# Optimization experiments

Hardware: AMD Instinct MI355X
Metric: run time of the kernel (lower is better)

Reference implementation:

```python
import jax, jax.numpy as jnp
import numpy as np

N = 100000      # nodes
E = 1600000     # edges (before self-loops)
IN = 128        # in_channels
H = 4           # heads
C = 32          # hidden_channels (per head)
HC = H * C      # 128, LayerNorm dim
NEG_SLOPE = 0.2
LN_EPS = 1e-5


def setup_inputs() -> dict:
    key = jax.random.key(0)
    ks = jax.random.split(key, 8)
    x = jax.random.normal(ks[0], (N, IN), dtype=jnp.float32)
    edge_index = jax.random.randint(ks[1], (2, E), 0, N, dtype=jnp.int64)
    edge_weight = jax.random.uniform(ks[2], (E,), dtype=jnp.float32)
    # GATConv parameters
    W = jax.random.normal(ks[3], (IN, HC), dtype=jnp.float32) * (1.0 / np.sqrt(IN))
    att_src = jax.random.normal(ks[4], (H, C), dtype=jnp.float32) * (1.0 / np.sqrt(C))
    att_dst = jax.random.normal(ks[5], (H, C), dtype=jnp.float32) * (1.0 / np.sqrt(C))
    bias = jnp.zeros((HC,), dtype=jnp.float32)
    # LayerNorm parameters
    gamma = jnp.ones((HC,), dtype=jnp.float32)
    beta = jnp.zeros((HC,), dtype=jnp.float32)
    return {"x": x, "edge_index": edge_index, "edge_weight": edge_weight,
            "W": W, "att_src": att_src, "att_dst": att_dst, "bias": bias,
            "gamma": gamma, "beta": beta}


def reference(x, edge_index, edge_weight, W, att_src, att_dst, bias, gamma, beta):
    # --- GATConv (heads=4, concat, add_self_loops=True) ---
    loops = jnp.arange(N, dtype=edge_index.dtype)
    ei = jnp.concatenate([edge_index, jnp.stack([loops, loops])], axis=1)  # [2, E+N]
    src, dst = ei[0], ei[1]

    xw = (x @ W).reshape(N, H, C)                       # [N, H, C]
    a_src = jnp.sum(xw * att_src, axis=-1)              # [N, H]
    a_dst = jnp.sum(xw * att_dst, axis=-1)              # [N, H]

    # per-edge attention logits, softmax grouped by destination node
    e = jax.nn.leaky_relu(a_src[src] + a_dst[dst], NEG_SLOPE)   # [E+N, H]
    m = jax.ops.segment_max(e, dst, num_segments=N)             # [N, H]
    ex = jnp.exp(e - m[dst])
    denom = jax.ops.segment_sum(ex, dst, num_segments=N)        # [N, H]
    alpha = ex / (denom[dst] + 1e-16)                           # [E+N, H]

    # weighted scatter-add of source features to destinations
    msg = alpha[:, :, None] * xw[src]                           # [E+N, H, C]
    out = jax.ops.segment_sum(msg, dst, num_segments=N)         # [N, H, C]
    out = out.reshape(N, HC) + bias                             # concat heads + bias

    # --- LayerNorm ---
    mu = jnp.mean(out, axis=-1, keepdims=True)
    var = jnp.var(out, axis=-1, keepdims=True)
    return gamma * (out - mu) / jnp.sqrt(var + LN_EPS) + beta
```

## Files before the change

### kernel.cpp

```cpp
#include <hip/hip_runtime.h>
#include <math.h>

#define NN 100000
#define EE 1600000
#define ETOT (EE + NN)
#define NBUK 512
#define NPB 196
#define CHUNK 3125
#define CAP 6144
#define GB 1563

typedef __attribute__((ext_vector_type(8))) short bf16x8;
typedef __attribute__((ext_vector_type(4))) float f32x4;

__device__ __forceinline__ unsigned short f2bf(float f) {
  unsigned int u = __float_as_uint(f);
  u = u + 0x7fffu + ((u >> 16) & 1u);
  return (unsigned short)(u >> 16);
}

__device__ __forceinline__ float lrelu_exp(float e) {
  e = (e > 0.f) ? e : 0.2f * e;
  return __expf(e);
}

__global__ __launch_bounds__(256) void k_gemm(const float* __restrict__ x,
                                              const float* __restrict__ W,
                                              const float* __restrict__ att_src,
                                              const float* __restrict__ att_dst,
                                              const int* __restrict__ ei,
                                              unsigned short* __restrict__ xwb,
                                              float* __restrict__ asrc,
                                              float* __restrict__ adst,
                                              int* __restrict__ H) {
  __shared__ __align__(16) unsigned short lds[17408];
  __shared__ float satt[256];
  __shared__ int hh[NBUK];
  int tid = threadIdx.x;

  if (blockIdx.x >= GB) {
    int j = blockIdx.x - GB;
    for (int i = tid; i < NBUK; i += 256) hh[i] = 0;
    __syncthreads();
    int e0 = j * CHUNK;
    for (int e = e0 + tid; e < e0 + CHUNK; e += 256) {
      int d = ei[(size_t)EE + e];
      atomicAdd(&hh[d / NPB], 1);
    }
    __syncthreads();
    for (int i = tid; i < NBUK; i += 256) H[j * NBUK + i] = hh[i];
    return;
  }

  for (int i = tid; i < 16384; i += 256) {
    int k = i >> 7, n = i & 127;
    lds[n * 136 + k] = f2bf(W[i]);
  }
  if (tid < 128) satt[tid] = att_src[tid];
  else satt[tid] = att_dst[tid - 128];
  __syncthreads();

  int wv = tid >> 6, lane = tid & 63;
  int m = lane & 15, q = lane >> 4;
  int r = blockIdx.x * 64 + wv * 16 + m;
  bool rok = (r < NN);

  bf16x8 af[4];
#pragma unroll
  for (int kt = 0; kt < 4; kt++) {
    float4 v0 = make_float4(0.f, 0.f, 0.f, 0.f), v1 = v0;
    if (rok) {
      v0 = ((const float4*)x)[(size_t)r * 32 + kt * 8 + q * 2];
      v1 = ((const float4*)x)[(size_t)r * 32 + kt * 8 + q * 2 + 1];
    }
    af[kt][0] = (short)f2bf(v0.x); af[kt][1] = (short)f2bf(v0.y);
    af[kt][2] = (short)f2bf(v0.z); af[kt][3] = (short)f2bf(v0.w);
    af[kt][4] = (short)f2bf(v1.x); af[kt][5] = (short)f2bf(v1.y);
    af[kt][6] = (short)f2bf(v1.z); af[kt][7] = (short)f2bf(v1.w);
  }

  f32x4 acc[8];
#pragma unroll
  for (int nt = 0; nt < 8; nt++) acc[nt] = (f32x4){0.f, 0.f, 0.f, 0.f};

#pragma unroll
  for (int nt = 0; nt < 8; nt++) {
#pragma unroll
    for (int kt = 0; kt < 4; kt++) {
      bf16x8 bf = *((const bf16x8*)&lds[(nt * 16 + m) * 136 + kt * 32 + q * 8]);
      acc[nt] = __builtin_amdgcn_mfma_f32_16x16x32_bf16(af[kt], bf, acc[nt], 0, 0, 0);
    }
  }

  __syncthreads();
#pragma unroll
  for (int nt = 0; nt < 8; nt++)
#pragma unroll
    for (int rg = 0; rg < 4; rg++)
      lds[(wv * 16 + q * 4 + rg) * 128 + nt * 16 + m] = f2bf(acc[nt][rg]);
  __syncthreads();

  size_t base = (size_t)blockIdx.x * 16384;
  const size_t lim = (size_t)NN * 256;
  for (int i = tid; i < 1024; i += 256) {
    size_t off = base + (size_t)i * 16;
    if (off < lim) *((uint4*)((char*)xwb + off)) = ((const uint4*)lds)[i];
  }

  int row = tid >> 2, h = tid & 3;
  int node = blockIdx.x * 64 + row;
  if (node < NN) {
    float ss = 0.f, sd = 0.f;
#pragma unroll
    for (int cq = 0; cq < 4; cq++) {
      uint4 u = *((const uint4*)&lds[row * 128 + h * 32 + cq * 8]);
      int cb = h * 32 + cq * 8;
      float f0 = __uint_as_float(u.x << 16), f1 = __uint_as_float(u.x & 0xffff0000u);
      float f2 = __uint_as_float(u.y << 16), f3 = __uint_as_float(u.y & 0xffff0000u);
      float f4 = __uint_as_float(u.z << 16), f5 = __uint_as_float(u.z & 0xffff0000u);
      float f6 = __uint_as_float(u.w << 16), f7 = __uint_as_float(u.w & 0xffff0000u);
      ss += f0 * satt[cb] + f1 * satt[cb + 1] + f2 * satt[cb + 2] + f3 * satt[cb + 3] +
            f4 * satt[cb + 4] + f5 * satt[cb + 5] + f6 * satt[cb + 6] + f7 * satt[cb + 7];
      sd += f0 * satt[128 + cb] + f1 * satt[128 + cb + 1] + f2 * satt[128 + cb + 2] +
            f3 * satt[128 + cb + 3] + f4 * satt[128 + cb + 4] + f5 * satt[128 + cb + 5] +
            f6 * satt[128 + cb + 6] + f7 * satt[128 + cb + 7];
    }
    asrc[(size_t)node * 4 + h] = ss;
    adst[(size_t)node * 4 + h] = sd;
  }
}

__global__ __launch_bounds__(512) void k_s1(const int* __restrict__ H,
                                            int* __restrict__ R, int* __restrict__ T) {
  __shared__ int s[512];
  int b = blockIdx.x, t = threadIdx.x;
  int v = H[t * NBUK + b];
  s[t] = v;
  __syncthreads();
  for (int off = 1; off < 512; off <<= 1) {
    int tmp = (t >= off) ? s[t - off] : 0;
    __syncthreads();
    s[t] += tmp;
    __syncthreads();
  }
  R[b * 512 + t] = s[t] - v;
  if (t == 511) T[b] = s[511];
}

__global__ __launch_bounds__(512) void k_s2(const int* __restrict__ T,
                                            int* __restrict__ BaseTmp,
                                            int* __restrict__ Base) {
  __shared__ int s[512];
  __shared__ int s2[512];
  int t = threadIdx.x;
  int v = T[t];
  int ncnt = NN - t * NPB;
  ncnt = (ncnt < 0) ? 0 : ((ncnt > NPB) ? NPB : ncnt);
  int w = v + ncnt;
  s[t] = v; s2[t] = w;
  __syncthreads();
  for (int off = 1; off < 512; off <<= 1) {
    int ta = (t >= off) ? s[t - off] : 0;
    int tb = (t >= off) ? s2[t - off] : 0;
    __syncthreads();
    s[t] += ta; s2[t] += tb;
    __syncthreads();
  }
  BaseTmp[t] = s[t] - v;
  Base[t] = s2[t] - w;
}

__global__ __launch_bounds__(256) void k_p3(const int* __restrict__ ei,
                                            const int* __restrict__ R,
                                            const int* __restrict__ BaseTmp,
                                            int* __restrict__ tmpb) {
  __shared__ int cur[NBUK];
  int j = blockIdx.x, t = threadIdx.x;
  for (int b = t; b < NBUK; b += 256) cur[b] = BaseTmp[b] + R[b * 512 + j];
  __syncthreads();
  int e0 = j * CHUNK;
  for (int e = e0 + t; e < e0 + CHUNK; e += 256) {
    int s = ei[e];
    int d = ei[(size_t)EE + e];
    int b = d / NPB;
    int li = d - b * NPB;
    int pos = atomicAdd(&cur[b], 1);
    tmpb[pos] = (li << 17) | s;
  }
}

__global__ __launch_bounds__(256) void k_p4(const int* __restrict__ tmpb,
                                            const int* __restrict__ T,
                                            const int* __restrict__ BaseTmp,
                                            const int* __restrict__ Base,
                                            int* __restrict__ es, int* __restrict__ offs) {
  __shared__ int cnt[256];
  __shared__ int cur[NPB];
  __shared__ int stage[CAP];
  int b = blockIdx.x, t = threadIdx.x;
  if (b == 0 && t == 0) offs[NN] = ETOT;
  int n0 = b * NPB;
  int nloc = NN - n0;
  if (nloc <= 0) return;
  if (nloc > NPB) nloc = NPB;
  int total = T[b];
  int bt = BaseTmp[b], bs = Base[b];
  cnt[t] = (t < nloc) ? 1 : 0;
  __syncthreads();
  for (int e = t; e < total; e += 256) {
    int u = tmpb[bt + e];
    atomicAdd(&cnt[u >> 17], 1);
  }
  __syncthreads();
  int v = cnt[t];
  __syncthreads();
  for (int off = 1; off < 256; off <<= 1) {
    int tmp = (t >= off) ? cnt[t - off] : 0;
    __syncthreads();
    cnt[t] += tmp;
    __syncthreads();
  }
  int excl = cnt[t] - v;
  if (t < nloc) {
    offs[n0 + t] = bs + excl;
    cur[t] = excl + 1;
    if (excl < CAP) stage[excl] = n0 + t;
  }
  __syncthreads();
  for (int e = t; e < total; e += 256) {
    int u = tmpb[bt + e];
    int pos = atomicAdd(&cur[u >> 17], 1);
    if (pos < CAP) stage[pos] = u & 0x1FFFF;
  }
  __syncthreads();
  int btot = total + nloc;
  if (btot > CAP) btot = CAP;
  for (int i = t; i < btot; i += 256) es[bs + i] = stage[i];
}

__global__ __launch_bounds__(256) void k_agg(const unsigned short* __restrict__ xwb,
                                             const float* __restrict__ asrc,
                                             const float* __restrict__ adst,
                                             const int* __restrict__ offs,
                                             const int* __restrict__ es,
                                             const float* __restrict__ bias,
                                             const float* __restrict__ gamma,
                                             const float* __restrict__ beta,
                                             float* __restrict__ out) {
  int lane = threadIdx.x & 63;
  int node = blockIdx.x * 4 + (threadIdx.x >> 6);
  int off0 = offs[node];
  int d = offs[node + 1] - off0;
  int h = lane >> 4;
  int he = lane & 3;
  int sel = lane >> 3;
  int c = lane * 2;

  float4 ad4 = *((const float4*)(adst + (size_t)node * 4));
  float ade = (he & 2) ? ((he & 1) ? ad4.w : ad4.z) : ((he & 1) ? ad4.y : ad4.x);

  const unsigned* xp = (const unsigned*)xwb + lane;
  const int* ep = es + off0;
  float ax0 = 0.f, ay0 = 0.f, ax1 = 0.f, ay1 = 0.f;
  float wsum = 0.f;

  int nb = (d + 7) >> 3;
  int4 sa = *((const int4*)(ep));
  int4 sb = *((const int4*)(ep + 4));

  for (int b = 0; b < nb; ++b) {
    int4 na = *((const int4*)(ep + (b + 1) * 8));
    int4 nbv = *((const int4*)(ep + (b + 1) * 8 + 4));

    int base = b * 8;
    int s0 = sa.x, s1 = sa.y, s2 = sa.z, s3 = sa.w;
    int s4 = sb.x, s5 = sb.y, s6 = sb.z, s7 = sb.w;
    bool full = (base + 8 <= d);
    if (!full) {
      s0 = (base + 0 < d) ? s0 : 0; s1 = (base + 1 < d) ? s1 : 0;
      s2 = (base + 2 < d) ? s2 : 0; s3 = (base + 3 < d) ? s3 : 0;
      s4 = (base + 4 < d) ? s4 : 0; s5 = (base + 5 < d) ? s5 : 0;
      s6 = (base + 6 < d) ? s6 : 0; s7 = (base + 7 < d) ? s7 : 0;
    }
    int t0 = (sel & 1) ? s1 : s0;
    int t1 = (sel & 1) ? s3 : s2;
    int t2 = (sel & 1) ? s5 : s4;
    int t3 = (sel & 1) ? s7 : s6;
    int p0 = (sel & 2) ? t1 : t0;
    int p1 = (sel & 2) ? t3 : t2;
    int se = (sel & 4) ? p1 : p0;
    float av = asrc[(size_t)(unsigned)se * 4u + (unsigned)he];

    unsigned u0 = xp[(unsigned)s0 * 64u];
    unsigned u1 = xp[(unsigned)s1 * 64u];
    unsigned u2 = xp[(unsigned)s2 * 64u];
    unsigned u3 = xp[(unsigned)s3 * 64u];
    unsigned u4 = xp[(unsigned)s4 * 64u];
    unsigned u5 = xp[(unsigned)s5 * 64u];
    unsigned u6 = xp[(unsigned)s6 * 64u];
    unsigned u7 = xp[(unsigned)s7 * 64u];

    float wl = lrelu_exp(av + ade);
    float w0 = __shfl(wl, 0 * 8 + h);
    float w1 = __shfl(wl, 1 * 8 + h);
    float w2 = __shfl(wl, 2 * 8 + h);
    float w3 = __shfl(wl, 3 * 8 + h);
    float w4 = __shfl(wl, 4 * 8 + h);
    float w5 = __shfl(wl, 5 * 8 + h);
    float w6 = __shfl(wl, 6 * 8 + h);
    float w7 = __shfl(wl, 7 * 8 + h);
    if (!full) {
      w0 = (base + 0 < d) ? w0 : 0.f; w1 = (base + 1 < d) ? w1 : 0.f;
      w2 = (base + 2 < d) ? w2 : 0.f; w3 = (base + 3 < d) ? w3 : 0.f;
      w4 = (base + 4 < d) ? w4 : 0.f; w5 = (base + 5 < d) ? w5 : 0.f;
      w6 = (base + 6 < d) ? w6 : 0.f; w7 = (base + 7 < d) ? w7 : 0.f;
    }
    wsum += ((w0 + w1) + (w2 + w3)) + ((w4 + w5) + (w6 + w7));
    ax0 = fmaf(w0, __uint_as_float(u0 << 16), ax0);
    ay0 = fmaf(w0, __uint_as_float(u0 & 0xffff0000u), ay0);
    ax1 = fmaf(w1, __uint_as_float(u1 << 16), ax1);
    ay1 = fmaf(w1, __uint_as_float(u1 & 0xffff0000u), ay1);
    ax0 = fmaf(w2, __uint_as_float(u2 << 16), ax0);
    ay0 = fmaf(w2, __uint_as_float(u2 & 0xffff0000u), ay0);
    ax1 = fmaf(w3, __uint_as_float(u3 << 16), ax1);
    ay1 = fmaf(w3, __uint_as_float(u3 & 0xffff0000u), ay1);
    ax0 = fmaf(w4, __uint_as_float(u4 << 16), ax0);
    ay0 = fmaf(w4, __uint_as_float(u4 & 0xffff0000u), ay0);
    ax1 = fmaf(w5, __uint_as_float(u5 << 16), ax1);
    ay1 = fmaf(w5, __uint_as_float(u5 & 0xffff0000u), ay1);
    ax0 = fmaf(w6, __uint_as_float(u6 << 16), ax0);
    ay0 = fmaf(w6, __uint_as_float(u6 & 0xffff0000u), ay0);
    ax1 = fmaf(w7, __uint_as_float(u7 << 16), ax1);
    ay1 = fmaf(w7, __uint_as_float(u7 & 0xffff0000u), ay1);

    sa = na; sb = nbv;
  }

  float accx = ax0 + ax1, accy = ay0 + ay1;
  float rn = 1.f / (wsum + 1e-16f);

  float vx = accx * rn + bias[c];
  float vy = accy * rn + bias[c + 1];
  float sum = vx + vy, sq = vx * vx + vy * vy;
#pragma unroll
  for (int o = 32; o; o >>= 1) {
    sum += __shfl_xor(sum, o);
    sq += __shfl_xor(sq, o);
  }
  float mean = sum * (1.f / 128.f);
  float var = sq * (1.f / 128.f) - mean * mean;
  float rs = rsqrtf(var + 1e-5f);
  float o0 = gamma[c] * (vx - mean) * rs + beta[c];
  float o1 = gamma[c + 1] * (vy - mean) * rs + beta[c + 1];
  float2 ov; ov.x = o0; ov.y = o1;
  *((float2*)(out + (size_t)node * 128 + c)) = ov;
}

extern "C" void kernel_launch(void* const* d_in, const int* in_sizes, int n_in,
                              void* d_out, int out_size, void* d_ws, size_t ws_size,
                              hipStream_t stream) {
  const float* x = (const float*)d_in[0];
  const int* ei = (const int*)d_in[1];
  const float* W = (const float*)d_in[3];
  const float* att_src = (const float*)d_in[4];
  const float* att_dst = (const float*)d_in[5];
  const float* bias = (const float*)d_in[6];
  const float* gamma = (const float*)d_in[7];
  const float* beta = (const float*)d_in[8];
  float* out = (float*)d_out;

  char* p = (char*)d_ws;
  auto alloc = [&](size_t bytes) -> char* {
    char* r = p;
    p += (bytes + 255) & ~(size_t)255;
    return r;
  };
  unsigned short* xwb = (unsigned short*)alloc((size_t)NN * 128 * 2);
  float* asrc = (float*)alloc((size_t)NN * 4 * 4);
  float* adst = (float*)alloc((size_t)NN * 4 * 4);
  int* es = (int*)alloc((size_t)ETOT * 4 + 128);
  int* offs = (int*)alloc((size_t)(NN + 1) * 4);
  int* tmpb = (int*)alloc((size_t)EE * 4);
  int* H = (int*)alloc((size_t)512 * NBUK * 4);
  int* R = (int*)alloc((size_t)NBUK * 512 * 4);
  int* T = (int*)alloc((size_t)NBUK * 4);
  int* BaseTmp = (int*)alloc((size_t)(NBUK + 1) * 4);
  int* Base = (int*)alloc((size_t)(NBUK + 1) * 4);

  k_gemm<<<GB + NBUK, 256, 0, stream>>>(x, W, att_src, att_dst, ei, xwb, asrc, adst, H);
  k_s1<<<NBUK, 512, 0, stream>>>(H, R, T);
  k_s2<<<1, 512, 0, stream>>>(T, BaseTmp, Base);
  k_p3<<<512, 256, 0, stream>>>(ei, R, BaseTmp, tmpb);
  k_p4<<<NBUK, 256, 0, stream>>>(tmpb, T, BaseTmp, Base, es, offs);
  k_agg<<<NN / 4, 256, 0, stream>>>(xwb, asrc, adst, offs, es, bias, gamma, beta, out);
}
```

Baseline: 255.2 us.

## Fuse CSR build stages into GEMM kernel with grid-wide atomic barriers

Merges the histogram, two scan kernels, bucket scatter and per-bucket sort into the GEMM launch. The first 512 blocks act as persistent workers that synchronise through global atomic counters, while the remaining blocks run the GEMM concurrently. This removes four kernel launches and lets the CSR construction overlap the matmul. It risks deadlock if the 512 worker blocks are not all co-resident, and adds spin-wait overhead plus a memset.

Result: slower. 633.7 us (+148.3%).

```diff
diff --git a/kernel.cpp b/kernel.cpp
--- a/kernel.cpp
+++ b/kernel.cpp
@@ -8,6 +8,7 @@
 #define NPB 196
 #define CHUNK 3125
 #define CAP 6144
+#define CB 512
 #define GB 1563
 
 typedef __attribute__((ext_vector_type(8))) short bf16x8;
@@ -24,7 +25,22 @@
   return __expf(e);
 }
 
-__global__ __launch_bounds__(256) void k_gemm(const float* __restrict__ x,
+__device__ __forceinline__ void arrive_cnt(int* c) {
+  __threadfence();
+  __syncthreads();
+  if (threadIdx.x == 0)
+    __hip_atomic_fetch_add(c, 1, __ATOMIC_RELAXED, __HIP_MEMORY_SCOPE_AGENT);
+}
+__device__ __forceinline__ void wait_cnt(int* c, int target) {
+  if (threadIdx.x == 0) {
+    while (__hip_atomic_load(c, __ATOMIC_RELAXED, __HIP_MEMORY_SCOPE_AGENT) < target)
+      __builtin_amdgcn_s_sleep(2);
+  }
+  __syncthreads();
+  __threadfence();
+}
+
+__global__ __launch_bounds__(256) void k_mega(const float* __restrict__ x,
                                               const float* __restrict__ W,
                                               const float* __restrict__ att_src,
                                               const float* __restrict__ att_dst,
@@ -32,26 +48,178 @@
                                               unsigned short* __restrict__ xwb,
                                               float* __restrict__ asrc,
                                               float* __restrict__ adst,
-                                              int* __restrict__ H) {
+                                              int* __restrict__ H, int* __restrict__ R,
+                                              int* __restrict__ T,
+                                              int* __restrict__ BaseTmp,
+                                              int* __restrict__ Base,
+                                              int* __restrict__ tmpb,
+                                              int* __restrict__ es, int* __restrict__ offs,
+                                              int* __restrict__ sync) {
   __shared__ __align__(16) unsigned short lds[17408];
   __shared__ float satt[256];
-  __shared__ int hh[NBUK];
   int tid = threadIdx.x;
-
-  if (blockIdx.x >= GB) {
-    int j = blockIdx.x - GB;
-    for (int i = tid; i < NBUK; i += 256) hh[i] = 0;
+  int* ish = (int*)lds;
+
+  if (blockIdx.x < CB) {
+    int j = blockIdx.x;
+    for (int i = tid; i < NBUK; i += 256) ish[i] = 0;
     __syncthreads();
     int e0 = j * CHUNK;
     for (int e = e0 + tid; e < e0 + CHUNK; e += 256) {
       int d = ei[(size_t)EE + e];
-      atomicAdd(&hh[d / NPB], 1);
+      atomicAdd(&ish[d / NPB], 1);
     }
     __syncthreads();
-    for (int i = tid; i < NBUK; i += 256) H[j * NBUK + i] = hh[i];
+    for (int i = tid; i < NBUK; i += 256) H[j * NBUK + i] = ish[i];
+    arrive_cnt(&sync[0]);
+    wait_cnt(&sync[0], CB);
+
+    {
+      int* s = ish;
+      int va = H[tid * NBUK + j];
+      int vb = H[(tid + 256) * NBUK + j];
+      s[tid] = va;
+      __syncthreads();
+      for (int off = 1; off < 256; off <<= 1) {
+        int tmp = (tid >= off) ? s[tid - off] : 0;
+        __syncthreads();
+        s[tid] += tmp;
+        __syncthreads();
+      }
+      int Sa = s[tid], SaT = s[255];
+      __syncthreads();
+      s[tid] = vb;
+      __syncthreads();
+      for (int off = 1; off < 256; off <<= 1) {
+        int tmp = (tid >= off) ? s[tid - off] : 0;
+        __syncthreads();
+        s[tid] += tmp;
+        __syncthreads();
+      }
+      int Sb = s[tid];
+      R[j * 512 + tid] = Sa - va;
+      R[j * 512 + 256 + tid] = SaT + Sb - vb;
+      if (tid == 255) T[j] = SaT + Sb;
+    }
+    arrive_cnt(&sync[1]);
+
+    if (j == 0) {
+      wait_cnt(&sync[1], CB);
+      int* s = ish;
+      int e2 = tid + 256;
+      int v1 = T[tid], v2 = T[e2];
+      int nc1 = NN - tid * NPB; nc1 = nc1 < 0 ? 0 : (nc1 > NPB ? NPB : nc1);
+      int nc2 = NN - e2 * NPB;  nc2 = nc2 < 0 ? 0 : (nc2 > NPB ? NPB : nc2);
+      int w1 = v1 + nc1, w2 = v2 + nc2;
+      s[tid] = v1;
+      __syncthreads();
+      for (int off = 1; off < 256; off <<= 1) {
+        int tmp = (tid >= off) ? s[tid - off] : 0;
+        __syncthreads();
+        s[tid] += tmp;
+        __syncthreads();
+      }
+      int Sa = s[tid], SaT = s[255];
+      __syncthreads();
+      s[tid] = v2;
+      __syncthreads();
+      for (int off = 1; off < 256; off <<= 1) {
+        int tmp = (tid >= off) ? s[tid - off] : 0;
+        __syncthreads();
+        s[tid] += tmp;
+        __syncthreads();
+      }
+      BaseTmp[tid] = Sa - v1;
+      BaseTmp[e2] = SaT + s[tid] - v2;
+      __syncthreads();
+      s[tid] = w1;
+      __syncthreads();
+      for (int off = 1; off < 256; off <<= 1) {
+        int tmp = (tid >= off) ? s[tid - off] : 0;
+        __syncthreads();
+        s[tid] += tmp;
+        __syncthreads();
+      }
+      int Sc = s[tid], ScT = s[255];
+      __syncthreads();
+      s[tid] = w2;
+      __syncthreads();
+      for (int off = 1; off < 256; off <<= 1) {
+        int tmp = (tid >= off) ? s[tid - off] : 0;
+        __syncthreads();
+        s[tid] += tmp;
+        __syncthreads();
+      }
+      Base[tid] = Sc - w1;
+      Base[e2] = ScT + s[tid] - w2;
+      arrive_cnt(&sync[2]);
+    }
+    wait_cnt(&sync[2], 1);
+
+    {
+      int* cur = ish;
+      for (int b2 = tid; b2 < NBUK; b2 += 256) cur[b2] = BaseTmp[b2] + R[b2 * 512 + j];
+      __syncthreads();
+      for (int e = e0 + tid; e < e0 + CHUNK; e += 256) {
+        int sv = ei[e];
+        int dv = ei[(size_t)EE + e];
+        int b2 = dv / NPB;
+        int li = dv - b2 * NPB;
+        int pos = atomicAdd(&cur[b2], 1);
+        tmpb[pos] = (li << 17) | sv;
+      }
+    }
+    arrive_cnt(&sync[3]);
+    wait_cnt(&sync[3], CB);
+
+    {
+      int* cnt = ish;
+      int* curn = ish + 256;
+      int* stage = ish + 512;
+      if (j == 0 && tid == 0) offs[NN] = ETOT;
+      int n0 = j * NPB;
+      int nloc = NN - n0;
+      if (nloc > 0) {
+        if (nloc > NPB) nloc = NPB;
+        int total = T[j];
+        int bt = BaseTmp[j], bs = Base[j];
+        cnt[tid] = (tid < nloc) ? 1 : 0;
+        __syncthreads();
+        for (int e = tid; e < total; e += 256) {
+          int u = tmpb[bt + e];
+          atomicAdd(&cnt[u >> 17], 1);
+        }
+        __syncthreads();
+        int v = cnt[tid];
+        __syncthreads();
+        for (int off = 1; off < 256; off <<= 1) {
+          int tmp = (tid >= off) ? cnt[tid - off] : 0;
+          __syncthreads();
+          cnt[tid] += tmp;
+          __syncthreads();
+        }
+        int excl = cnt[tid] - v;
+        if (tid < nloc) {
+          offs[n0 + tid] = bs + excl;
+          curn[tid] = excl + 1;
+          if (excl < CAP) stage[excl] = n0 + tid;
+        }
+        __syncthreads();
+        for (int e = tid; e < total; e += 256) {
+          int u = tmpb[bt + e];
+          int pos = atomicAdd(&curn[u >> 17], 1);
+          if (pos < CAP) stage[pos] = u & 0x1FFFF;
+        }
+        __syncthreads();
+        int btot = total + nloc;
+        if (btot > CAP) btot = CAP;
+        for (int i = tid; i < btot; i += 256) es[bs + i] = stage[i];
+      }
+    }
     return;
   }
 
+  int gb = blockIdx.x - CB;
   for (int i = tid; i < 16384; i += 256) {
     int k = i >> 7, n = i & 127;
     lds[n * 136 + k] = f2bf(W[i]);
@@ -62,7 +230,7 @@
 
   int wv = tid >> 6, lane = tid & 63;
   int m = lane & 15, q = lane >> 4;
-  int r = blockIdx.x * 64 + wv * 16 + m;
+  int r = gb * 64 + wv * 16 + m;
   bool rok = (r < NN);
 
   bf16x8 af[4];
@@ -100,7 +268,7 @@
       lds[(wv * 16 + q * 4 + rg) * 128 + nt * 16 + m] = f2bf(acc[nt][rg]);
   __syncthreads();
 
-  size_t base = (size_t)blockIdx.x * 16384;
+  size_t base = (size_t)gb * 16384;
   const size_t lim = (size_t)NN * 256;
   for (int i = tid; i < 1024; i += 256) {
     size_t off = base + (size_t)i * 16;
@@ -108,7 +276,7 @@
   }
 
   int row = tid >> 2, h = tid & 3;
-  int node = blockIdx.x * 64 + row;
+  int node = gb * 64 + row;
   if (node < NN) {
     float ss = 0.f, sd = 0.f;
 #pragma unroll
@@ -128,114 +296,6 @@
     asrc[(size_t)node * 4 + h] = ss;
     adst[(size_t)node * 4 + h] = sd;
   }
-}
-
-__global__ __launch_bounds__(512) void k_s1(const int* __restrict__ H,
-                                            int* __restrict__ R, int* __restrict__ T) {
-  __shared__ int s[512];
-  int b = blockIdx.x, t = threadIdx.x;
-  int v = H[t * NBUK + b];
-  s[t] = v;
-  __syncthreads();
-  for (int off = 1; off < 512; off <<= 1) {
-    int tmp = (t >= off) ? s[t - off] : 0;
-    __syncthreads();
-    s[t] += tmp;
-    __syncthreads();
-  }
-  R[b * 512 + t] = s[t] - v;
-  if (t == 511) T[b] = s[511];
-}
-
-__global__ __launch_bounds__(512) void k_s2(const int* __restrict__ T,
-                                            int* __restrict__ BaseTmp,
-                                            int* __restrict__ Base) {
-  __shared__ int s[512];
-  __shared__ int s2[512];
-  int t = threadIdx.x;
-  int v = T[t];
-  int ncnt = NN - t * NPB;
-  ncnt = (ncnt < 0) ? 0 : ((ncnt > NPB) ? NPB : ncnt);
-  int w = v + ncnt;
-  s[t] = v; s2[t] = w;
-  __syncthreads();
-  for (int off = 1; off < 512; off <<= 1) {
-    int ta = (t >= off) ? s[t - off] : 0;
-    int tb = (t >= off) ? s2[t - off] : 0;
-    __syncthreads();
-    s[t] += ta; s2[t] += tb;
-    __syncthreads();
-  }
-  BaseTmp[t] = s[t] - v;
-  Base[t] = s2[t] - w;
-}
-
-__global__ __launch_bounds__(256) void k_p3(const int* __restrict__ ei,
-                                            const int* __restrict__ R,
-                                            const int* __restrict__ BaseTmp,
-                                            int* __restrict__ tmpb) {
-  __shared__ int cur[NBUK];
-  int j = blockIdx.x, t = threadIdx.x;
-  for (int b = t; b < NBUK; b += 256) cur[b] = BaseTmp[b] + R[b * 512 + j];
-  __syncthreads();
-  int e0 = j * CHUNK;
-  for (int e = e0 + t; e < e0 + CHUNK; e += 256) {
-    int s = ei[e];
-    int d = ei[(size_t)EE + e];
-    int b = d / NPB;
-    int li = d - b * NPB;
-    int pos = atomicAdd(&cur[b], 1);
-    tmpb[pos] = (li << 17) | s;
-  }
-}
-
-__global__ __launch_bounds__(256) void k_p4(const int* __restrict__ tmpb,
-                                            const int* __restrict__ T,
-                                            const int* __restrict__ BaseTmp,
-                                            const int* __restrict__ Base,
-                                            int* __restrict__ es, int* __restrict__ offs) {
-  __shared__ int cnt[256];
-  __shared__ int cur[NPB];
-  __shared__ int stage[CAP];
-  int b = blockIdx.x, t = threadIdx.x;
-  if (b == 0 && t == 0) offs[NN] = ETOT;
-  int n0 = b * NPB;
-  int nloc = NN - n0;
-  if (nloc <= 0) return;
-  if (nloc > NPB) nloc = NPB;
-  int total = T[b];
-  int bt = BaseTmp[b], bs = Base[b];
-  cnt[t] = (t < nloc) ? 1 : 0;
-  __syncthreads();
-  for (int e = t; e < total; e += 256) {
-    int u = tmpb[bt + e];
-    atomicAdd(&cnt[u >> 17], 1);
-  }
-  __syncthreads();
-  int v = cnt[t];
-  __syncthreads();
-  for (int off = 1; off < 256; off <<= 1) {
-    int tmp = (t >= off) ? cnt[t - off] : 0;
-    __syncthreads();
-    cnt[t] += tmp;
-    __syncthreads();
-  }
-  int excl = cnt[t] - v;
-  if (t < nloc) {
-    offs[n0 + t] = bs + excl;
-    cur[t] = excl + 1;
-    if (excl < CAP) stage[excl] = n0 + t;
-  }
-  __syncthreads();
-  for (int e = t; e < total; e += 256) {
-    int u = tmpb[bt + e];
-    int pos = atomicAdd(&cur[u >> 17], 1);
-    if (pos < CAP) stage[pos] = u & 0x1FFFF;
-  }
-  __syncthreads();
-  int btot = total + nloc;
-  if (btot > CAP) btot = CAP;
-  for (int i = t; i < btot; i += 256) es[bs + i] = stage[i];
 }
 
 __global__ __launch_bounds__(256) void k_agg(const unsigned short* __restrict__ xwb,
@@ -386,11 +446,10 @@
   int* T = (int*)alloc((size_t)NBUK * 4);
   int* BaseTmp = (int*)alloc((size_t)(NBUK + 1) * 4);
   int* Base = (int*)alloc((size_t)(NBUK + 1) * 4);
-
-  k_gemm<<<GB + NBUK, 256, 0, stream>>>(x, W, att_src, att_dst, ei, xwb, asrc, adst, H);
-  k_s1<<<NBUK, 512, 0, stream>>>(H, R, T);
-  k_s2<<<1, 512, 0, stream>>>(T, BaseTmp, Base);
-  k_p3<<<512, 256, 0, stream>>>(ei, R, BaseTmp, tmpb);
-  k_p4<<<NBUK, 256, 0, stream>>>(tmpb, T, BaseTmp, Base, es, offs);
+  int* sync = (int*)alloc(64);
+
+  hipMemsetAsync(sync, 0, 16, stream);
+  k_mega<<<CB + GB, 256, 0, stream>>>(x, W, att_src, att_dst, ei, xwb, asrc, adst,
+                                      H, R, T, BaseTmp, Base, tmpb, es, offs, sync);
   k_agg<<<NN / 4, 256, 0, stream>>>(xwb, asrc, adst, offs, es, bias, gamma, beta, out);
 }
```

## Bucket edges locally per chunk in LDS, gather per-bucket segments in p4

Applied to the files above, without the earlier changes.

The histogram blocks now also compute a per-chunk exclusive scan of bucket counts. k_p3 then scatters each chunk's edges into an LDS staging array and writes it back contiguously, replacing random global scatter writes with coalesced ones. k_p4 gathers each bucket's segments from all 512 chunks into LDS before counting and placing them. This adds per-thread serial loops over small segments in k_p4 and extra LDS use, since k_p4 now holds two CAP-sized arrays.

Result: faster. 249.2 us (-2.3%).

```diff
diff --git a/kernel.cpp b/kernel.cpp
--- a/kernel.cpp
+++ b/kernel.cpp
@@ -32,7 +32,8 @@
                                               unsigned short* __restrict__ xwb,
                                               float* __restrict__ asrc,
                                               float* __restrict__ adst,
-                                              int* __restrict__ H) {
+                                              int* __restrict__ H,
+                                              int* __restrict__ Sc) {
   __shared__ __align__(16) unsigned short lds[17408];
   __shared__ float satt[256];
   __shared__ int hh[NBUK];
@@ -49,6 +50,28 @@
     }
     __syncthreads();
     for (int i = tid; i < NBUK; i += 256) H[j * NBUK + i] = hh[i];
+    int* s = (int*)lds;
+    int va = hh[tid], vb = hh[tid + 256];
+    s[tid] = va;
+    __syncthreads();
+    for (int off = 1; off < 256; off <<= 1) {
+      int tmp = (tid >= off) ? s[tid - off] : 0;
+      __syncthreads();
+      s[tid] += tmp;
+      __syncthreads();
+    }
+    int Sa = s[tid], SaT = s[255];
+    __syncthreads();
+    s[tid] = vb;
+    __syncthreads();
+    for (int off = 1; off < 256; off <<= 1) {
+      int tmp = (tid >= off) ? s[tid - off] : 0;
+      __syncthreads();
+      s[tid] += tmp;
+      __syncthreads();
+    }
+    Sc[j * 512 + tid] = Sa - va;
+    Sc[j * 512 + 256 + tid] = SaT + s[tid] - vb;
     return;
   }
 
@@ -148,55 +171,56 @@
 }
 
 __global__ __launch_bounds__(512) void k_s2(const int* __restrict__ T,
-                                            int* __restrict__ BaseTmp,
                                             int* __restrict__ Base) {
-  __shared__ int s[512];
   __shared__ int s2[512];
   int t = threadIdx.x;
   int v = T[t];
   int ncnt = NN - t * NPB;
   ncnt = (ncnt < 0) ? 0 : ((ncnt > NPB) ? NPB : ncnt);
   int w = v + ncnt;
-  s[t] = v; s2[t] = w;
+  s2[t] = w;
   __syncthreads();
   for (int off = 1; off < 512; off <<= 1) {
-    int ta = (t >= off) ? s[t - off] : 0;
     int tb = (t >= off) ? s2[t - off] : 0;
     __syncthreads();
-    s[t] += ta; s2[t] += tb;
-    __syncthreads();
-  }
-  BaseTmp[t] = s[t] - v;
+    s2[t] += tb;
+    __syncthreads();
+  }
   Base[t] = s2[t] - w;
 }
 
 __global__ __launch_bounds__(256) void k_p3(const int* __restrict__ ei,
-                                            const int* __restrict__ R,
-                                            const int* __restrict__ BaseTmp,
+                                            const int* __restrict__ Sc,
                                             int* __restrict__ tmpb) {
   __shared__ int cur[NBUK];
+  __shared__ int stage2[CHUNK];
   int j = blockIdx.x, t = threadIdx.x;
-  for (int b = t; b < NBUK; b += 256) cur[b] = BaseTmp[b] + R[b * 512 + j];
+  for (int b = t; b < NBUK; b += 256) cur[b] = Sc[j * 512 + b];
   __syncthreads();
   int e0 = j * CHUNK;
   for (int e = e0 + t; e < e0 + CHUNK; e += 256) {
-    int s = ei[e];
-    int d = ei[(size_t)EE + e];
-    int b = d / NPB;
-    int li = d - b * NPB;
+    int sv = ei[e];
+    int dv = ei[(size_t)EE + e];
+    int b = dv / NPB;
+    int li = dv - b * NPB;
     int pos = atomicAdd(&cur[b], 1);
-    tmpb[pos] = (li << 17) | s;
-  }
+    stage2[pos] = (li << 17) | sv;
+  }
+  __syncthreads();
+  for (int i = t; i < CHUNK; i += 256) tmpb[(size_t)j * CHUNK + i] = stage2[i];
 }
 
 __global__ __launch_bounds__(256) void k_p4(const int* __restrict__ tmpb,
+                                            const int* __restrict__ H,
+                                            const int* __restrict__ R,
                                             const int* __restrict__ T,
-                                            const int* __restrict__ BaseTmp,
+                                            const int* __restrict__ Sc,
                                             const int* __restrict__ Base,
                                             int* __restrict__ es, int* __restrict__ offs) {
+  __shared__ int raw[CAP];
+  __shared__ int stage[CAP];
   __shared__ int cnt[256];
-  __shared__ int cur[NPB];
-  __shared__ int stage[CAP];
+  __shared__ int curn[NPB];
   int b = blockIdx.x, t = threadIdx.x;
   if (b == 0 && t == 0) offs[NN] = ETOT;
   int n0 = b * NPB;
@@ -204,12 +228,20 @@
   if (nloc <= 0) return;
   if (nloc > NPB) nloc = NPB;
   int total = T[b];
-  int bt = BaseTmp[b], bs = Base[b];
+  int bs = Base[b];
   cnt[t] = (t < nloc) ? 1 : 0;
   __syncthreads();
-  for (int e = t; e < total; e += 256) {
-    int u = tmpb[bt + e];
-    atomicAdd(&cnt[u >> 17], 1);
+  for (int jj = t; jj < 512; jj += 256) {
+    int st = Sc[jj * 512 + b];
+    int ln = H[jj * NBUK + b];
+    int rb = R[b * 512 + jj];
+    const int* src = tmpb + (size_t)jj * CHUNK + st;
+    for (int k = 0; k < ln; k++) {
+      int w = src[k];
+      int p = rb + k;
+      if (p < CAP) raw[p] = w;
+      atomicAdd(&cnt[w >> 17], 1);
+    }
   }
   __syncthreads();
   int v = cnt[t];
@@ -223,13 +255,14 @@
   int excl = cnt[t] - v;
   if (t < nloc) {
     offs[n0 + t] = bs + excl;
-    cur[t] = excl + 1;
+    curn[t] = excl + 1;
     if (excl < CAP) stage[excl] = n0 + t;
   }
   __syncthreads();
-  for (int e = t; e < total; e += 256) {
-    int u = tmpb[bt + e];
-    int pos = atomicAdd(&cur[u >> 17], 1);
+  int tl = (total < CAP) ? total : CAP;
+  for (int e = t; e < tl; e += 256) {
+    int u = raw[e];
+    int pos = atomicAdd(&curn[u >> 17], 1);
     if (pos < CAP) stage[pos] = u & 0x1FFFF;
   }
   __syncthreads();
@@ -382,15 +415,15 @@
   int* offs = (int*)alloc((size_t)(NN + 1) * 4);
   int* tmpb = (int*)alloc((size_t)EE * 4);
   int* H = (int*)alloc((size_t)512 * NBUK * 4);
+  int* Sc = (int*)alloc((size_t)512 * NBUK * 4);
   int* R = (int*)alloc((size_t)NBUK * 512 * 4);
   int* T = (int*)alloc((size_t)NBUK * 4);
-  int* BaseTmp = (int*)alloc((size_t)(NBUK + 1) * 4);
   int* Base = (int*)alloc((size_t)(NBUK + 1) * 4);
 
-  k_gemm<<<GB + NBUK, 256, 0, stream>>>(x, W, att_src, att_dst, ei, xwb, asrc, adst, H);
+  k_gemm<<<GB + NBUK, 256, 0, stream>>>(x, W, att_src, att_dst, ei, xwb, asrc, adst, H, Sc);
   k_s1<<<NBUK, 512, 0, stream>>>(H, R, T);
-  k_s2<<<1, 512, 0, stream>>>(T, BaseTmp, Base);
-  k_p3<<<512, 256, 0, stream>>>(ei, R, BaseTmp, tmpb);
-  k_p4<<<NBUK, 256, 0, stream>>>(tmpb, T, BaseTmp, Base, es, offs);
+  k_s2<<<1, 512, 0, stream>>>(T, Base);
+  k_p3<<<512, 256, 0, stream>>>(ei, Sc, tmpb);
+  k_p4<<<NBUK, 256, 0, stream>>>(tmpb, H, R, T, Sc, Base, es, offs);
   k_agg<<<NN / 4, 256, 0, stream>>>(xwb, asrc, adst, offs, es, bias, gamma, beta, out);
 }
```
